# Kernel tuning notes

Hardware: AMD Instinct MI355X
Metric: run time of the kernel (lower is better)

## Reference

```python
import jax, jax.numpy as jnp
import numpy as np

B, N, D = 2, 4096, 1024
DS = 1024           # state_dim (defaults to embed_dim)
H = 4096            # mlp hidden = int(embed_dim * 4.0)
EPS = 1e-5


def _layernorm(x, w, b):
    mu = jnp.mean(x, axis=-1, keepdims=True)
    var = jnp.mean((x - mu) ** 2, axis=-1, keepdims=True)
    return (x - mu) * jax.lax.rsqrt(var + EPS) * w + b


def _selective_scan(deltaA, deltaB_u):
    # deltaA: (B, N, 1), deltaB_u: (B, N, DS). Recurrence h_i = dA_i * h + dBu_i.
    def step(h, inp):
        dA, dBu = inp           # (B,1), (B,DS)
        h = dA * h + dBu
        return h, h
    h0 = jnp.zeros((deltaB_u.shape[0], deltaB_u.shape[2]), deltaB_u.dtype)
    _, ys = jax.lax.scan(step, h0,
                         (jnp.swapaxes(deltaA, 0, 1), jnp.swapaxes(deltaB_u, 0, 1)))
    return jnp.swapaxes(ys, 0, 1)   # (B, N, DS)


def _forward(x, norm1_w, norm1_b, gate_w, gate_b, state_w, state_b,
             out_w, out_b, norm2_w, norm2_b, mlp_w1, mlp_b1, mlp_w2, mlp_b2):
    xn = _layernorm(x, norm1_w, norm1_b)
    g = xn @ gate_w + gate_b                       # (B,N,2D)
    gate, gate_gate = jnp.split(g, 2, axis=-1)
    gate = jax.nn.silu(gate)
    gate_gate = jax.nn.silu(gate_gate)
    u = (xn * gate) @ state_w + state_b            # (B,N,DS)
    Bm = gate_gate @ state_w + state_b             # (B,N,DS)
    # A = -ones(DS) -> delta*A = -delta broadcast over DS; keep (B,N,1)
    delta = jax.nn.softplus(jnp.mean(xn @ state_w + state_b, axis=-1, keepdims=True))
    deltaA = jnp.exp(-delta)                       # (B,N,1)
    deltaB_u = delta * Bm * u                      # (B,N,DS)
    # C = ones -> y_i = C_i * h_i = h_i
    y = _selective_scan(deltaA, deltaB_u)
    ssm_out = y @ out_w + out_b
    x = x + ssm_out
    x2 = _layernorm(x, norm2_w, norm2_b)
    mlp = jax.nn.gelu(x2 @ mlp_w1 + mlp_b1, approximate=False) @ mlp_w2 + mlp_b2
    return x + mlp


def setup_inputs() -> dict:
    key = jax.random.key(0)
    ks = jax.random.split(key, 12)
    s = 0.02
    p = lambda k, shape: jax.random.normal(k, shape, jnp.float32) * s
    return {
        "x": jax.random.normal(ks[0], (B, N, D), jnp.float32),
        "norm1_w": jnp.ones((D,), jnp.float32), "norm1_b": jnp.zeros((D,), jnp.float32),
        "gate_w": p(ks[1], (D, 2 * D)), "gate_b": p(ks[2], (2 * D,)),
        "state_w": p(ks[3], (D, DS)), "state_b": p(ks[4], (DS,)),
        "out_w": p(ks[5], (DS, D)), "out_b": p(ks[6], (D,)),
        "norm2_w": jnp.ones((D,), jnp.float32), "norm2_b": jnp.zeros((D,), jnp.float32),
        "mlp_w1": p(ks[7], (D, H)), "mlp_b1": p(ks[8], (H,)),
        "mlp_w2": p(ks[9], (H, D)), "mlp_b2": p(ks[10], (D,)),
    }


def reference(x, norm1_w, norm1_b, gate_w, gate_b, state_w, state_b,
              out_w, out_b, norm2_w, norm2_b, mlp_w1, mlp_b1, mlp_w2, mlp_b2):
    return _forward(x, norm1_w, norm1_b, gate_w, gate_b, state_w, state_b,
                    out_w, out_b, norm2_w, norm2_b, mlp_w1, mlp_b1, mlp_w2, mlp_b2)
```

## Files before the change

### kernel.cpp

```cpp
#include <hip/hip_runtime.h>
#include <hip/hip_bf16.h>
#include <math.h>

#define B_   2
#define N_   4096
#define D_   1024
#define DS_  1024
#define HID_ 4096
#define ROWS (B_ * N_)

#define CHK 128
#define TCH 32

typedef __attribute__((ext_vector_type(8))) short bf16x8;
typedef __attribute__((ext_vector_type(4))) float f32x4;

#define ASG __attribute__((address_space(1)))
#define AS3 __attribute__((address_space(3)))

__device__ __forceinline__ float bf2f(unsigned short u) {
  union { float f; unsigned int i; } v; v.i = ((unsigned int)u) << 16; return v.f;
}
__device__ __forceinline__ unsigned short f2bf(float f) {
  union { float f; unsigned int i; } v; v.f = f;
  unsigned int r = v.i + 0x7fffu + ((v.i >> 16) & 1u);
  return (unsigned short)(r >> 16);
}

__global__ void means_kernel(const float* __restrict__ W, const float* __restrict__ bvec,
                             float* __restrict__ swmean, float* __restrict__ sbmean) {
  __shared__ float sm[4];
  int bid = blockIdx.x, t = threadIdx.x;
  const float* src = (bid < D_) ? (W + (size_t)bid * DS_) : bvec;
  float s = 0.f;
  for (int j = t; j < DS_; j += 256) s += src[j];
  for (int o = 32; o; o >>= 1) s += __shfl_down(s, o);
  if ((t & 63) == 0) sm[t >> 6] = s;
  __syncthreads();
  if (t == 0) {
    float r = (sm[0] + sm[1] + sm[2] + sm[3]) * (1.f / DS_);
    if (bid < D_) swmean[bid] = r; else sbmean[0] = r;
  }
}

__global__ void transpose_bf16_kernel(const float* __restrict__ W, unsigned short* __restrict__ WT,
                                      int K, int N) {
  __shared__ float tile[32][33];
  int tx = threadIdx.x & 31, ty = threadIdx.x >> 5;
  int bn = blockIdx.x * 32, bk = blockIdx.y * 32;
  for (int i = ty; i < 32; i += 8)
    tile[i][tx] = W[(size_t)(bk + i) * N + bn + tx];
  __syncthreads();
  for (int i = ty; i < 32; i += 8)
    WT[(size_t)(bn + i) * K + bk + tx] = f2bf(tile[tx][i]);
}

template<bool WITH_DELTA>
__global__ void ln_kernel(const float* __restrict__ x, const float* __restrict__ w,
                          const float* __restrict__ bb, unsigned short* __restrict__ out_bf,
                          const float* __restrict__ swmean, const float* __restrict__ sbmean,
                          float* __restrict__ delta) {
  __shared__ float sm[8];
  __shared__ float bc[2];
  int row = blockIdx.x, t = threadIdx.x;
  const float* xr = x + (size_t)row * D_;
  float4 xv = ((const float4*)xr)[t];
  float s  = xv.x + xv.y + xv.z + xv.w;
  float sq = xv.x * xv.x + xv.y * xv.y + xv.z * xv.z + xv.w * xv.w;
  for (int o = 32; o; o >>= 1) { s += __shfl_down(s, o); sq += __shfl_down(sq, o); }
  if ((t & 63) == 0) { sm[t >> 6] = s; sm[4 + (t >> 6)] = sq; }
  __syncthreads();
  if (t == 0) {
    float ts = sm[0] + sm[1] + sm[2] + sm[3];
    float tq = sm[4] + sm[5] + sm[6] + sm[7];
    float mu = ts * (1.f / D_);
    float var = tq * (1.f / D_) - mu * mu;
    bc[0] = mu; bc[1] = rsqrtf(var + 1e-5f);
  }
  __syncthreads();
  float mu = bc[0], rs = bc[1];
  float4 wv = ((const float4*)w)[t];
  float4 bv = ((const float4*)bb)[t];
  float n0 = (xv.x - mu) * rs * wv.x + bv.x;
  float n1 = (xv.y - mu) * rs * wv.y + bv.y;
  float n2 = (xv.z - mu) * rs * wv.z + bv.z;
  float n3 = (xv.w - mu) * rs * wv.w + bv.w;
  ushort4 o4; o4.x = f2bf(n0); o4.y = f2bf(n1); o4.z = f2bf(n2); o4.w = f2bf(n3);
  ((ushort4*)(out_bf + (size_t)row * D_))[t] = o4;
  if (WITH_DELTA) {
    float4 sw = ((const float4*)swmean)[t];
    float d = n0 * sw.x + n1 * sw.y + n2 * sw.z + n3 * sw.w;
    for (int o = 32; o; o >>= 1) d += __shfl_down(d, o);
    if ((t & 63) == 0) sm[t >> 6] = d;
    __syncthreads();
    if (t == 0) {
      float z = sm[0] + sm[1] + sm[2] + sm[3] + sbmean[0];
      delta[row] = (z > 15.f) ? z : log1pf(__expf(z));
    }
  }
}


#define BARX { __builtin_amdgcn_s_barrier(); __builtin_amdgcn_sched_barrier(0); }

#define RD_A(TAU, H) { const char* ab_ = smem + ((((TAU)&1)*2+(H))<<14); \
  _Pragma("unroll") for (int mm_ = 0; mm_ < MB_H; ++mm_) \
  _Pragma("unroll") for (int ks_ = 0; ks_ < 2; ++ks_) { \
    int r_ = wr*(16*MB_H) + mm_*16 + l15; \
    int by_ = r_*128 + ks_*64 + kq16; by_ ^= ((by_>>7)&7)<<4; \
    af[mm_][ks_] = *(const bf16x8*)(ab_ + by_); } }

#define RD_B(TAU, H, DST) { const char* bb_ = smemB + ((((TAU)&1)*2+(H)))*SB; \
  _Pragma("unroll") for (int nn_ = 0; nn_ < NB_H; ++nn_) \
  _Pragma("unroll") for (int ks_ = 0; ks_ < 2; ++ks_) { \
    int r_ = wc*(16*NB_H) + nn_*16 + l15; \
    int by_ = r_*128 + ks_*64 + kq16; by_ ^= ((by_>>7)&7)<<4; \
    DST[nn_][ks_] = *(const bf16x8*)(bb_ + by_); } }

#define MFMAQ(QA, QB, BF) { __builtin_amdgcn_s_setprio(1); \
  _Pragma("unroll") for (int m_ = 0; m_ < MB_H; ++m_) \
  _Pragma("unroll") for (int n_ = 0; n_ < NB_H; ++n_) \
  _Pragma("unroll") for (int k_ = 0; k_ < 2; ++k_) \
    acc[(QA)*MB_H+m_][(QB)*NB_H+n_] = __builtin_amdgcn_mfma_f32_16x16x32_bf16( \
        af[m_][k_], BF[n_][k_], acc[(QA)*MB_H+m_][(QB)*NB_H+n_], 0, 0, 0); \
  __builtin_amdgcn_s_setprio(0); }

template<int BN, int EPI>
__global__ __launch_bounds__(512, 2) void gemm8p(
    const unsigned short* __restrict__ A1p, int lda1, int M1,
    const unsigned short* __restrict__ A2p, int lda2,
    const unsigned short* __restrict__ BT, const float* __restrict__ bias,
    void* __restrict__ Cout, const float* __restrict__ res,
    int N, int K, int nbx) {
  constexpr int WN   = (BN == 256) ? 4 : 2;
  constexpr int MB_H = (BN == 256) ? 4 : 2;
  constexpr int NB_H = 2;
  constexpr int MF   = 2 * MB_H;
  constexpr int LB   = BN / 128;
  constexpr int SB   = (BN / 2) * 64 * 2;
  __shared__ char smem[65536 + 4 * SB];
  char* smemB = smem + 65536;

  const int nwg = gridDim.x;
  int bid = blockIdx.x;
  int wg = (bid & 7) * (nwg >> 3) + (bid >> 3);
  const int bx = wg % nbx, by = wg / nbx;
  const int mbase = by * 256, nbase = bx * BN;

  const int tid = threadIdx.x;
  const int lane = tid & 63, wid = tid >> 6;
  const int wr = wid / WN, wc = wid % WN;
  const int l15 = lane & 15, kq16 = (lane >> 4) * 16;
  const int wvoff16 = wid << 10;

  const unsigned short* Ause; int ldaU;
  if (mbase < M1) { Ause = A1p + (size_t)mbase * lda1; ldaU = lda1; }
  else            { Ause = A2p + (size_t)(mbase - M1) * lda2; ldaU = lda2; }

  int L0 = tid * 16;        int b0 = L0 ^ (((L0 >> 7) & 7) << 4);
  int L1 = 8192 + tid * 16; int b1 = L1 ^ (((L1 >> 7) & 7) << 4);
  const unsigned short* pA0 = Ause + (size_t)(b0 >> 7) * ldaU + ((b0 & 127) >> 1);
  const unsigned short* pA1 = Ause + (size_t)(b1 >> 7) * ldaU + ((b1 & 127) >> 1);
  const unsigned short* pB0 = BT + (size_t)(nbase + (b0 >> 7)) * K + ((b0 & 127) >> 1);
  const unsigned short* pB1 = BT + (size_t)(nbase + (b1 >> 7)) * K + ((b1 & 127) >> 1);

  auto stageA = [&](int tau, int h, bool en) {
    if (!en) return;
    char* l0 = smem + (((tau & 1) * 2 + h) << 14) + wvoff16;
    const unsigned short* g0 = pA0 + (size_t)h * 128 * ldaU + tau * 64;
    const unsigned short* g1 = pA1 + (size_t)h * 128 * ldaU + tau * 64;
    __builtin_amdgcn_global_load_lds((const ASG void*)g0, (AS3 void*)l0, 16, 0, 0);
    __builtin_amdgcn_global_load_lds((const ASG void*)g1, (AS3 void*)(l0 + 8192), 16, 0, 0);
  };
  auto stageB = [&](int tau, int h, bool en) {
    if (!en) return;
    char* l0 = smemB + ((tau & 1) * 2 + h) * SB + wvoff16;
    const unsigned short* g0 = pB0 + (size_t)h * (BN / 2) * K + tau * 64;
    __builtin_amdgcn_global_load_lds((const ASG void*)g0, (AS3 void*)l0, 16, 0, 0);
    if constexpr (LB == 2) {
      const unsigned short* g1 = pB1 + (size_t)h * (BN / 2) * K + tau * 64;
      __builtin_amdgcn_global_load_lds((const ASG void*)g1, (AS3 void*)(l0 + 8192), 16, 0, 0);
    }
  };
  auto vm_steady = [&]() {
    if constexpr (BN == 256) { asm volatile("s_waitcnt vmcnt(6)" ::: "memory"); }
    else                     { asm volatile("s_waitcnt vmcnt(5)" ::: "memory"); }
  };

  f32x4 acc[MF][4];
#pragma unroll
  for (int m = 0; m < MF; ++m)
#pragma unroll
    for (int n = 0; n < 4; ++n) acc[m][n] = (f32x4){0.f, 0.f, 0.f, 0.f};
  bf16x8 af[MB_H][2], bq0[NB_H][2], bq1[NB_H][2];

  const int NT = K >> 6, NI = NT >> 1;

  stageA(0, 0, true); stageB(0, 0, true); stageA(0, 1, true); stageB(0, 1, true);
  stageA(1, 0, true); stageB(1, 0, true); stageA(1, 1, true);
  vm_steady();
  BARX;

#pragma unroll 1
  for (int i = 0; i < NI; ++i) {
    const int t0 = 2 * i;
    const bool st = (i < NI - 1);
    RD_A(t0, 0); RD_B(t0, 0, bq0); stageB(t0 + 1, 1, true);
    BARX; MFMAQ(0, 0, bq0); BARX;
    RD_B(t0, 1, bq1); stageA(t0 + 2, 0, st);
    BARX; MFMAQ(0, 1, bq1); BARX;
    RD_A(t0, 1); stageB(t0 + 2, 0, st);
    BARX; MFMAQ(1, 1, bq1); BARX;
    stageA(t0 + 2, 1, st);
    if (st) { vm_steady(); } else { asm volatile("s_waitcnt vmcnt(0)" ::: "memory"); }
    BARX; MFMAQ(1, 0, bq0); BARX;
    RD_A(t0 + 1, 0); RD_B(t0 + 1, 0, bq0); stageB(t0 + 2, 1, st);
    BARX; MFMAQ(0, 0, bq0); BARX;
    RD_B(t0 + 1, 1, bq1); stageA(t0 + 3, 0, st);
    BARX; MFMAQ(0, 1, bq1); BARX;
    RD_A(t0 + 1, 1); stageB(t0 + 3, 0, st);
    BARX; MFMAQ(1, 1, bq1); BARX;
    stageA(t0 + 3, 1, st);
    if (st) vm_steady();
    BARX; MFMAQ(1, 0, bq0); BARX;
  }

#pragma unroll
  for (int mb = 0; mb < MF; ++mb) {
    int row = mbase + wr * (16 * MB_H) + (mb % MB_H) * 16 + (mb / MB_H) * 128 + (lane >> 4) * 4;
#pragma unroll
    for (int nb = 0; nb < 4; ++nb) {
      int col = nbase + wc * (16 * NB_H) + (nb % NB_H) * 16 + (nb / NB_H) * (BN / 2) + l15;
      float bc = bias[col];
#pragma unroll
      for (int r = 0; r < 4; ++r) {
        float v = acc[mb][nb][r] + bc;
        size_t off = (size_t)(row + r) * N + col;
        if (EPI == 1) {
          v = v / (1.f + __expf(-v));
          ((unsigned short*)Cout)[off] = f2bf(v);
        } else if (EPI == 2) {
          ((unsigned short*)Cout)[off] = f2bf(v);
        } else if (EPI == 3) {
          ((float*)Cout)[off] = v + res[off];
        } else if (EPI == 4) {
          float tt = v * (0.7978845608f + 0.0356774081f * v * v);
          v = v / (1.f + __expf(-2.f * tt));
          ((unsigned short*)Cout)[off] = f2bf(v);
        }
      }
    }
  }
}

__global__ void ew_xg_kernel(const unsigned short* __restrict__ xn,
                             const unsigned short* __restrict__ gs,
                             unsigned short* __restrict__ xg) {
  size_t i8 = ((size_t)blockIdx.x * 256 + threadIdx.x) * 8;
  size_t row = i8 >> 10, col = i8 & 1023;
  uint4 xv = *(const uint4*)(xn + i8);
  uint4 gv = *(const uint4*)(gs + row * 2048 + col);
  const unsigned short* xs = (const unsigned short*)&xv;
  const unsigned short* gg = (const unsigned short*)&gv;
  uint4 ov; unsigned short* o = (unsigned short*)&ov;
#pragma unroll
  for (int j = 0; j < 8; ++j) o[j] = f2bf(bf2f(xs[j]) * bf2f(gg[j]));
  *(uint4*)(xg + i8) = ov;
}

__global__ void ew_dbu_kernel(const unsigned short* __restrict__ u,
                              const unsigned short* __restrict__ bm,
                              const float* __restrict__ delta,
                              unsigned short* __restrict__ dbu) {
  size_t i8 = ((size_t)blockIdx.x * 256 + threadIdx.x) * 8;
  size_t row = i8 >> 10;
  float dl = delta[row];
  uint4 uv = *(const uint4*)(u + i8);
  uint4 bv = *(const uint4*)(bm + i8);
  const unsigned short* us = (const unsigned short*)&uv;
  const unsigned short* bs = (const unsigned short*)&bv;
  uint4 ov; unsigned short* o = (unsigned short*)&ov;
#pragma unroll
  for (int j = 0; j < 8; ++j) o[j] = f2bf(dl * bf2f(us[j]) * bf2f(bs[j]));
  *(uint4*)(dbu + i8) = ov;
}

__global__ void scan_a_kernel(const unsigned short* __restrict__ dbu,
                              const float* __restrict__ delta,
                              float* __restrict__ hend, float* __restrict__ S) {
  int blk = blockIdx.x;
  int b = blk / CHK, c = blk % CHK;
  int ch = threadIdx.x;
  const unsigned short* p = dbu + ((size_t)(b * N_ + c * TCH)) * DS_ + ch;
  const float* dp = delta + b * N_ + c * TCH;
  float h = 0.f, dsum = 0.f;
#pragma unroll 4
  for (int t = 0; t < TCH; ++t) {
    float dl = dp[t];
    h = __expf(-dl) * h + bf2f(p[(size_t)t * DS_]);
    dsum += dl;
  }
  hend[(size_t)blk * DS_ + ch] = h;
  if (ch == 0) S[blk] = dsum;
}

__global__ void scan_combine_kernel(const float* __restrict__ hend, const float* __restrict__ S,
                                    float* __restrict__ carryin) {
  int b = blockIdx.x, ch = threadIdx.x;
  float carry = 0.f;
  for (int c = 0; c < CHK; ++c) {
    size_t o = (size_t)(b * CHK + c) * DS_ + ch;
    carryin[o] = carry;
    carry = __expf(-S[b * CHK + c]) * carry + hend[o];
  }
}

__global__ void scan_b_kernel(const unsigned short* __restrict__ dbu,
                              const float* __restrict__ delta,
                              const float* __restrict__ carryin,
                              unsigned short* __restrict__ y) {
  int blk = blockIdx.x;
  int b = blk / CHK, c = blk % CHK;
  int ch = threadIdx.x;
  size_t base = ((size_t)(b * N_ + c * TCH)) * DS_ + ch;
  const float* dp = delta + b * N_ + c * TCH;
  float h = carryin[(size_t)blk * DS_ + ch];
#pragma unroll 4
  for (int t = 0; t < TCH; ++t) {
    h = __expf(-dp[t]) * h + bf2f(dbu[base + (size_t)t * DS_]);
    y[base + (size_t)t * DS_] = f2bf(h);
  }
}

extern "C" void kernel_launch(void* const* d_in, const int* in_sizes, int n_in,
                              void* d_out, int out_size, void* d_ws, size_t ws_size,
                              hipStream_t stream) {
  const float* x       = (const float*)d_in[0];
  const float* n1w     = (const float*)d_in[1];
  const float* n1b     = (const float*)d_in[2];
  const float* gate_w  = (const float*)d_in[3];
  const float* gate_b  = (const float*)d_in[4];
  const float* state_w = (const float*)d_in[5];
  const float* state_b = (const float*)d_in[6];
  const float* out_w   = (const float*)d_in[7];
  const float* out_b   = (const float*)d_in[8];
  const float* n2w     = (const float*)d_in[9];
  const float* n2b     = (const float*)d_in[10];
  const float* mlp_w1  = (const float*)d_in[11];
  const float* mlp_b1  = (const float*)d_in[12];
  const float* mlp_w2  = (const float*)d_in[13];
  const float* mlp_b2  = (const float*)d_in[14];
  float* outp = (float*)d_out;

  char* w = (char*)d_ws;
  size_t off = 0;
  auto alloc = [&](size_t bytes) { char* p = w + off; off += (bytes + 255) & ~(size_t)255; return p; };

  unsigned short* gate_wT  = (unsigned short*)alloc((size_t)2048 * 1024 * 2);
  unsigned short* state_wT = (unsigned short*)alloc((size_t)1024 * 1024 * 2);
  unsigned short* out_wT   = (unsigned short*)alloc((size_t)1024 * 1024 * 2);
  unsigned short* w1T      = (unsigned short*)alloc((size_t)4096 * 1024 * 2);
  unsigned short* w2T      = (unsigned short*)alloc((size_t)1024 * 4096 * 2);
  float* swmean  = (float*)alloc(D_ * 4);
  float* sbmean  = (float*)alloc(256);
  float* delta   = (float*)alloc((size_t)ROWS * 4);
  float* hend    = (float*)alloc((size_t)B_ * CHK * DS_ * 4);
  float* carryin = (float*)alloc((size_t)B_ * CHK * DS_ * 4);
  float* S       = (float*)alloc((size_t)B_ * CHK * 4);
  unsigned short* xn = (unsigned short*)alloc((size_t)ROWS * D_ * 2);
  unsigned short* gs = (unsigned short*)alloc((size_t)ROWS * HID_ * 2);
  unsigned short* xg = (unsigned short*)alloc((size_t)ROWS * D_ * 2);
  float* x1          = (float*)alloc((size_t)ROWS * D_ * 4);

  unsigned short* dbu = xn;
  unsigned short* h1  = gs;
  unsigned short* y   = xg;
  unsigned short* x2  = xg;
  unsigned short* u   = (unsigned short*)x1;
  unsigned short* bm  = u + (size_t)ROWS * D_;

  means_kernel<<<D_ + 1, 256, 0, stream>>>(state_w, state_b, swmean, sbmean);
  transpose_bf16_kernel<<<dim3(2048 / 32, 1024 / 32), 256, 0, stream>>>(gate_w, gate_wT, 1024, 2048);
  transpose_bf16_kernel<<<dim3(1024 / 32, 1024 / 32), 256, 0, stream>>>(state_w, state_wT, 1024, 1024);
  transpose_bf16_kernel<<<dim3(1024 / 32, 1024 / 32), 256, 0, stream>>>(out_w, out_wT, 1024, 1024);
  transpose_bf16_kernel<<<dim3(4096 / 32, 1024 / 32), 256, 0, stream>>>(mlp_w1, w1T, 1024, 4096);
  transpose_bf16_kernel<<<dim3(1024 / 32, 4096 / 32), 256, 0, stream>>>(mlp_w2, w2T, 4096, 1024);

  ln_kernel<true><<<ROWS, 256, 0, stream>>>(x, n1w, n1b, xn, swmean, sbmean, delta);

  const int BIG = 1 << 30;
  gemm8p<256, 1><<<256, 512, 0, stream>>>(xn, 1024, BIG, xn, 1024,
                                          gate_wT, gate_b, gs, nullptr, 2048, 1024, 8);
  ew_xg_kernel<<<(ROWS * D_) / 8 / 256, 256, 0, stream>>>(xn, gs, xg);
  gemm8p<256, 2><<<256, 512, 0, stream>>>(xg, 1024, 8192, gs + 1024, 2048,
                                          state_wT, state_b, u, nullptr, 1024, 1024, 4);
  ew_dbu_kernel<<<(ROWS * D_) / 8 / 256, 256, 0, stream>>>(u, bm, delta, dbu);

  scan_a_kernel<<<B_ * CHK, 1024, 0, stream>>>(dbu, delta, hend, S);
  scan_combine_kernel<<<B_, 1024, 0, stream>>>(hend, S, carryin);
  scan_b_kernel<<<B_ * CHK, 1024, 0, stream>>>(dbu, delta, carryin, y);

  gemm8p<128, 3><<<256, 512, 0, stream>>>(y, 1024, BIG, y, 1024,
                                          out_wT, out_b, x1, x, 1024, 1024, 8);
  ln_kernel<false><<<ROWS, 256, 0, stream>>>(x1, n2w, n2b, x2, nullptr, nullptr, nullptr);
  gemm8p<256, 4><<<512, 512, 0, stream>>>(x2, 1024, BIG, x2, 1024,
                                          w1T, mlp_b1, h1, nullptr, 4096, 1024, 16);
  gemm8p<128, 3><<<256, 512, 0, stream>>>(h1, 4096, BIG, h1, 4096,
                                          w2T, mlp_b2, outp, x1, 1024, 4096, 8);
}
```

Measured before the change: 367.4 us.

## Fuse xn*gate product into gate GEMM epilogue and relax barrier scheduling

Adds an EPI==5 epilogue to the gate GEMM that applies SiLU and writes the first half multiplied by xn directly into xg, and the second half as a compact 1024-wide gate_gate buffer. This removes the separate ew_xg kernel and the 2048-wide gs round trip, and the state GEMM now reads a contiguous gate_gate array. It also drops sched_barrier from the barrier macro and issues global stage loads before the LDS reads in each phase, letting the compiler interleave instructions more freely. The risk is that the compiler reorders LDS reads or MFMAs across the barriers in ways that hurt the hand-tuned pipeline.

Result: slower. 392.9 us (+6.9%).

```diff
diff --git a/kernel.cpp b/kernel.cpp
--- a/kernel.cpp
+++ b/kernel.cpp
@@ -101,7 +101,7 @@
 }
 
 
-#define BARX { __builtin_amdgcn_s_barrier(); __builtin_amdgcn_sched_barrier(0); }
+#define BAR __builtin_amdgcn_s_barrier()
 
 #define RD_A(TAU, H) { const char* ab_ = smem + ((((TAU)&1)*2+(H))<<14); \
   _Pragma("unroll") for (int mm_ = 0; mm_ < MB_H; ++mm_) \
@@ -131,7 +131,7 @@
     const unsigned short* __restrict__ A2p, int lda2,
     const unsigned short* __restrict__ BT, const float* __restrict__ bias,
     void* __restrict__ Cout, const float* __restrict__ res,
-    int N, int K, int nbx) {
+    int N, int K, int nbx, void* __restrict__ Cout2) {
   constexpr int WN   = (BN == 256) ? 4 : 2;
   constexpr int MB_H = (BN == 256) ? 4 : 2;
   constexpr int NB_H = 2;
@@ -199,30 +199,30 @@
   stageA(0, 0, true); stageB(0, 0, true); stageA(0, 1, true); stageB(0, 1, true);
   stageA(1, 0, true); stageB(1, 0, true); stageA(1, 1, true);
   vm_steady();
-  BARX;
+  BAR;
 
 #pragma unroll 1
   for (int i = 0; i < NI; ++i) {
     const int t0 = 2 * i;
     const bool st = (i < NI - 1);
-    RD_A(t0, 0); RD_B(t0, 0, bq0); stageB(t0 + 1, 1, true);
-    BARX; MFMAQ(0, 0, bq0); BARX;
-    RD_B(t0, 1, bq1); stageA(t0 + 2, 0, st);
-    BARX; MFMAQ(0, 1, bq1); BARX;
-    RD_A(t0, 1); stageB(t0 + 2, 0, st);
-    BARX; MFMAQ(1, 1, bq1); BARX;
+    stageB(t0 + 1, 1, true); RD_A(t0, 0); RD_B(t0, 0, bq0);
+    BAR; MFMAQ(0, 0, bq0); BAR;
+    stageA(t0 + 2, 0, st); RD_B(t0, 1, bq1);
+    BAR; MFMAQ(0, 1, bq1); BAR;
+    stageB(t0 + 2, 0, st); RD_A(t0, 1);
+    BAR; MFMAQ(1, 1, bq1); BAR;
     stageA(t0 + 2, 1, st);
     if (st) { vm_steady(); } else { asm volatile("s_waitcnt vmcnt(0)" ::: "memory"); }
-    BARX; MFMAQ(1, 0, bq0); BARX;
-    RD_A(t0 + 1, 0); RD_B(t0 + 1, 0, bq0); stageB(t0 + 2, 1, st);
-    BARX; MFMAQ(0, 0, bq0); BARX;
-    RD_B(t0 + 1, 1, bq1); stageA(t0 + 3, 0, st);
-    BARX; MFMAQ(0, 1, bq1); BARX;
-    RD_A(t0 + 1, 1); stageB(t0 + 3, 0, st);
-    BARX; MFMAQ(1, 1, bq1); BARX;
+    BAR; MFMAQ(1, 0, bq0); BAR;
+    stageB(t0 + 2, 1, st); RD_A(t0 + 1, 0); RD_B(t0 + 1, 0, bq0);
+    BAR; MFMAQ(0, 0, bq0); BAR;
+    stageA(t0 + 3, 0, st); RD_B(t0 + 1, 1, bq1);
+    BAR; MFMAQ(0, 1, bq1); BAR;
+    stageB(t0 + 3, 0, st); RD_A(t0 + 1, 1);
+    BAR; MFMAQ(1, 1, bq1); BAR;
     stageA(t0 + 3, 1, st);
     if (st) vm_steady();
-    BARX; MFMAQ(1, 0, bq0); BARX;
+    BAR; MFMAQ(1, 0, bq0); BAR;
   }
 
 #pragma unroll
@@ -247,25 +247,20 @@
           float tt = v * (0.7978845608f + 0.0356774081f * v * v);
           v = v / (1.f + __expf(-2.f * tt));
           ((unsigned short*)Cout)[off] = f2bf(v);
+        } else if (EPI == 5) {
+          float s = v / (1.f + __expf(-v));
+          if (col < 1024) {
+            size_t o1 = (size_t)(row + r) * 1024 + col;
+            float xv = bf2f(((const unsigned short*)res)[o1]);
+            ((unsigned short*)Cout)[o1] = f2bf(s * xv);
+          } else {
+            size_t o2 = (size_t)(row + r) * 1024 + (col - 1024);
+            ((unsigned short*)Cout2)[o2] = f2bf(s);
+          }
         }
       }
     }
   }
-}
-
-__global__ void ew_xg_kernel(const unsigned short* __restrict__ xn,
-                             const unsigned short* __restrict__ gs,
-                             unsigned short* __restrict__ xg) {
-  size_t i8 = ((size_t)blockIdx.x * 256 + threadIdx.x) * 8;
-  size_t row = i8 >> 10, col = i8 & 1023;
-  uint4 xv = *(const uint4*)(xn + i8);
-  uint4 gv = *(const uint4*)(gs + row * 2048 + col);
-  const unsigned short* xs = (const unsigned short*)&xv;
-  const unsigned short* gg = (const unsigned short*)&gv;
-  uint4 ov; unsigned short* o = (unsigned short*)&ov;
-#pragma unroll
-  for (int j = 0; j < 8; ++j) o[j] = f2bf(bf2f(xs[j]) * bf2f(gg[j]));
-  *(uint4*)(xg + i8) = ov;
 }
 
 __global__ void ew_dbu_kernel(const unsigned short* __restrict__ u,
@@ -372,12 +367,13 @@
   unsigned short* xg = (unsigned short*)alloc((size_t)ROWS * D_ * 2);
   float* x1          = (float*)alloc((size_t)ROWS * D_ * 4);
 
-  unsigned short* dbu = xn;
-  unsigned short* h1  = gs;
-  unsigned short* y   = xg;
-  unsigned short* x2  = xg;
-  unsigned short* u   = (unsigned short*)x1;
-  unsigned short* bm  = u + (size_t)ROWS * D_;
+  unsigned short* dbu   = xn;
+  unsigned short* gsil2 = gs;
+  unsigned short* h1    = gs;
+  unsigned short* y     = xg;
+  unsigned short* x2    = xg;
+  unsigned short* u     = (unsigned short*)x1;
+  unsigned short* bm    = u + (size_t)ROWS * D_;
 
   means_kernel<<<D_ + 1, 256, 0, stream>>>(state_w, state_b, swmean, sbmean);
   transpose_bf16_kernel<<<dim3(2048 / 32, 1024 / 32), 256, 0, stream>>>(gate_w, gate_wT, 1024, 2048);
@@ -389,11 +385,10 @@
   ln_kernel<true><<<ROWS, 256, 0, stream>>>(x, n1w, n1b, xn, swmean, sbmean, delta);
 
   const int BIG = 1 << 30;
-  gemm8p<256, 1><<<256, 512, 0, stream>>>(xn, 1024, BIG, xn, 1024,
-                                          gate_wT, gate_b, gs, nullptr, 2048, 1024, 8);
-  ew_xg_kernel<<<(ROWS * D_) / 8 / 256, 256, 0, stream>>>(xn, gs, xg);
-  gemm8p<256, 2><<<256, 512, 0, stream>>>(xg, 1024, 8192, gs + 1024, 2048,
-                                          state_wT, state_b, u, nullptr, 1024, 1024, 4);
+  gemm8p<256, 5><<<256, 512, 0, stream>>>(xn, 1024, BIG, xn, 1024,
+                                          gate_wT, gate_b, xg, (const float*)xn, 2048, 1024, 8, gsil2);
+  gemm8p<256, 2><<<256, 512, 0, stream>>>(xg, 1024, 8192, gsil2, 1024,
+                                          state_wT, state_b, u, nullptr, 1024, 1024, 4, nullptr);
   ew_dbu_kernel<<<(ROWS * D_) / 8 / 256, 256, 0, stream>>>(u, bm, delta, dbu);
 
   scan_a_kernel<<<B_ * CHK, 1024, 0, stream>>>(dbu, delta, hend, S);
@@ -401,10 +396,10 @@
   scan_b_kernel<<<B_ * CHK, 1024, 0, stream>>>(dbu, delta, carryin, y);
 
   gemm8p<128, 3><<<256, 512, 0, stream>>>(y, 1024, BIG, y, 1024,
-                                          out_wT, out_b, x1, x, 1024, 1024, 8);
+                                          out_wT, out_b, x1, x, 1024, 1024, 8, nullptr);
   ln_kernel<false><<<ROWS, 256, 0, stream>>>(x1, n2w, n2b, x2, nullptr, nullptr, nullptr);
   gemm8p<256, 4><<<512, 512, 0, stream>>>(x2, 1024, BIG, x2, 1024,
-                                          w1T, mlp_b1, h1, nullptr, 4096, 1024, 16);
+                                          w1T, mlp_b1, h1, nullptr, 4096, 1024, 16, nullptr);
   gemm8p<128, 3><<<256, 512, 0, stream>>>(h1, 4096, BIG, h1, 4096,
-                                          w2T, mlp_b2, outp, x1, 1024, 4096, 8);
-}
+                                          w2T, mlp_b2, outp, x1, 1024, 4096, 8, nullptr);
+}
```

## Fuse delta*B*u into scan kernels and make MLP1 GEMM persistent over two tiles

Applied to the files above, without the earlier changes.

The elementwise dbu kernel is removed. Both scan passes now read u and Bm directly and compute delta*Bm*u inline, which saves one full write and read of an intermediate. The MLP up-projection GEMM gets a P2 mode in which each of 256 workgroups computes two M tiles back to back, continuing the load pipeline across the tile boundary and running the epilogue in between. The sched_barrier after each s_barrier is also dropped, giving the compiler more scheduling freedom but possibly disturbing the hand-tuned interleave; the scans now read two bf16 streams instead of one.

Measured after the change: 406.5 us. 10.6% more time.

```diff
diff --git a/kernel.cpp b/kernel.cpp
--- a/kernel.cpp
+++ b/kernel.cpp
@@ -101,7 +101,7 @@
 }
 
 
-#define BARX { __builtin_amdgcn_s_barrier(); __builtin_amdgcn_sched_barrier(0); }
+#define BAR __builtin_amdgcn_s_barrier()
 
 #define RD_A(TAU, H) { const char* ab_ = smem + ((((TAU)&1)*2+(H))<<14); \
   _Pragma("unroll") for (int mm_ = 0; mm_ < MB_H; ++mm_) \
@@ -125,7 +125,7 @@
         af[m_][k_], BF[n_][k_], acc[(QA)*MB_H+m_][(QB)*NB_H+n_], 0, 0, 0); \
   __builtin_amdgcn_s_setprio(0); }
 
-template<int BN, int EPI>
+template<int BN, int EPI, bool P2>
 __global__ __launch_bounds__(512, 2) void gemm8p(
     const unsigned short* __restrict__ A1p, int lda1, int M1,
     const unsigned short* __restrict__ A2p, int lda2,
@@ -146,6 +146,7 @@
   int wg = (bid & 7) * (nwg >> 3) + (bid >> 3);
   const int bx = wg % nbx, by = wg / nbx;
   const int mbase = by * 256, nbase = bx * BN;
+  const int mstep = (nwg / nbx) * 256;
 
   const int tid = threadIdx.x;
   const int lane = tid & 63, wid = tid >> 6;
@@ -156,6 +157,7 @@
   const unsigned short* Ause; int ldaU;
   if (mbase < M1) { Ause = A1p + (size_t)mbase * lda1; ldaU = lda1; }
   else            { Ause = A2p + (size_t)(mbase - M1) * lda2; ldaU = lda2; }
+  const size_t A2off = (size_t)mstep * ldaU;
 
   int L0 = tid * 16;        int b0 = L0 ^ (((L0 >> 7) & 7) << 4);
   int L1 = 8192 + tid * 16; int b1 = L1 ^ (((L1 >> 7) & 7) << 4);
@@ -164,17 +166,27 @@
   const unsigned short* pB0 = BT + (size_t)(nbase + (b0 >> 7)) * K + ((b0 & 127) >> 1);
   const unsigned short* pB1 = BT + (size_t)(nbase + (b1 >> 7)) * K + ((b1 & 127) >> 1);
 
-  auto stageA = [&](int tau, int h, bool en) {
-    if (!en) return;
-    char* l0 = smem + (((tau & 1) * 2 + h) << 14) + wvoff16;
-    const unsigned short* g0 = pA0 + (size_t)h * 128 * ldaU + tau * 64;
-    const unsigned short* g1 = pA1 + (size_t)h * 128 * ldaU + tau * 64;
+  const int KT  = K >> 6;
+  const int NI1 = KT >> 1;
+  const int NTV = P2 ? 2 * KT : KT;
+  const int NIV = P2 ? 2 * NI1 : NI1;
+
+  auto stageA = [&](int tau, int h) {
+    if (tau >= NTV) return;
+    int slot = tau & 1;
+    const unsigned short *a0 = pA0, *a1 = pA1;
+    if (P2 && tau >= KT) { tau -= KT; a0 += A2off; a1 += A2off; }
+    char* l0 = smem + ((slot * 2 + h) << 14) + wvoff16;
+    const unsigned short* g0 = a0 + (size_t)h * 128 * ldaU + tau * 64;
+    const unsigned short* g1 = a1 + (size_t)h * 128 * ldaU + tau * 64;
     __builtin_amdgcn_global_load_lds((const ASG void*)g0, (AS3 void*)l0, 16, 0, 0);
     __builtin_amdgcn_global_load_lds((const ASG void*)g1, (AS3 void*)(l0 + 8192), 16, 0, 0);
   };
-  auto stageB = [&](int tau, int h, bool en) {
-    if (!en) return;
-    char* l0 = smemB + ((tau & 1) * 2 + h) * SB + wvoff16;
+  auto stageB = [&](int tau, int h) {
+    if (tau >= NTV) return;
+    int slot = tau & 1;
+    if (P2 && tau >= KT) tau -= KT;
+    char* l0 = smemB + (slot * 2 + h) * SB + wvoff16;
     const unsigned short* g0 = pB0 + (size_t)h * (BN / 2) * K + tau * 64;
     __builtin_amdgcn_global_load_lds((const ASG void*)g0, (AS3 void*)l0, 16, 0, 0);
     if constexpr (LB == 2) {
@@ -194,63 +206,72 @@
     for (int n = 0; n < 4; ++n) acc[m][n] = (f32x4){0.f, 0.f, 0.f, 0.f};
   bf16x8 af[MB_H][2], bq0[NB_H][2], bq1[NB_H][2];
 
-  const int NT = K >> 6, NI = NT >> 1;
-
-  stageA(0, 0, true); stageB(0, 0, true); stageA(0, 1, true); stageB(0, 1, true);
-  stageA(1, 0, true); stageB(1, 0, true); stageA(1, 1, true);
-  vm_steady();
-  BARX;
-
-#pragma unroll 1
-  for (int i = 0; i < NI; ++i) {
-    const int t0 = 2 * i;
-    const bool st = (i < NI - 1);
-    RD_A(t0, 0); RD_B(t0, 0, bq0); stageB(t0 + 1, 1, true);
-    BARX; MFMAQ(0, 0, bq0); BARX;
-    RD_B(t0, 1, bq1); stageA(t0 + 2, 0, st);
-    BARX; MFMAQ(0, 1, bq1); BARX;
-    RD_A(t0, 1); stageB(t0 + 2, 0, st);
-    BARX; MFMAQ(1, 1, bq1); BARX;
-    stageA(t0 + 2, 1, st);
-    if (st) { vm_steady(); } else { asm volatile("s_waitcnt vmcnt(0)" ::: "memory"); }
-    BARX; MFMAQ(1, 0, bq0); BARX;
-    RD_A(t0 + 1, 0); RD_B(t0 + 1, 0, bq0); stageB(t0 + 2, 1, st);
-    BARX; MFMAQ(0, 0, bq0); BARX;
-    RD_B(t0 + 1, 1, bq1); stageA(t0 + 3, 0, st);
-    BARX; MFMAQ(0, 1, bq1); BARX;
-    RD_A(t0 + 1, 1); stageB(t0 + 3, 0, st);
-    BARX; MFMAQ(1, 1, bq1); BARX;
-    stageA(t0 + 3, 1, st);
-    if (st) vm_steady();
-    BARX; MFMAQ(1, 0, bq0); BARX;
-  }
-
-#pragma unroll
-  for (int mb = 0; mb < MF; ++mb) {
-    int row = mbase + wr * (16 * MB_H) + (mb % MB_H) * 16 + (mb / MB_H) * 128 + (lane >> 4) * 4;
-#pragma unroll
-    for (int nb = 0; nb < 4; ++nb) {
-      int col = nbase + wc * (16 * NB_H) + (nb % NB_H) * 16 + (nb / NB_H) * (BN / 2) + l15;
-      float bc = bias[col];
-#pragma unroll
-      for (int r = 0; r < 4; ++r) {
-        float v = acc[mb][nb][r] + bc;
-        size_t off = (size_t)(row + r) * N + col;
-        if (EPI == 1) {
-          v = v / (1.f + __expf(-v));
-          ((unsigned short*)Cout)[off] = f2bf(v);
-        } else if (EPI == 2) {
-          ((unsigned short*)Cout)[off] = f2bf(v);
-        } else if (EPI == 3) {
-          ((float*)Cout)[off] = v + res[off];
-        } else if (EPI == 4) {
-          float tt = v * (0.7978845608f + 0.0356774081f * v * v);
-          v = v / (1.f + __expf(-2.f * tt));
-          ((unsigned short*)Cout)[off] = f2bf(v);
+  auto epi = [&](int tile) {
+    const int moff = P2 ? tile * mstep : 0;
+#pragma unroll
+    for (int mb = 0; mb < MF; ++mb) {
+      int row = mbase + moff + wr * (16 * MB_H) + (mb % MB_H) * 16 + (mb / MB_H) * 128 + (lane >> 4) * 4;
+#pragma unroll
+      for (int nb = 0; nb < 4; ++nb) {
+        int col = nbase + wc * (16 * NB_H) + (nb % NB_H) * 16 + (nb / NB_H) * (BN / 2) + l15;
+        float bc = bias[col];
+#pragma unroll
+        for (int r = 0; r < 4; ++r) {
+          float v = acc[mb][nb][r] + bc;
+          size_t off = (size_t)(row + r) * N + col;
+          if (EPI == 1) {
+            v = v / (1.f + __expf(-v));
+            ((unsigned short*)Cout)[off] = f2bf(v);
+          } else if (EPI == 2) {
+            ((unsigned short*)Cout)[off] = f2bf(v);
+          } else if (EPI == 3) {
+            ((float*)Cout)[off] = v + res[off];
+          } else if (EPI == 4) {
+            float tt = v * (0.7978845608f + 0.0356774081f * v * v);
+            v = v / (1.f + __expf(-2.f * tt));
+            ((unsigned short*)Cout)[off] = f2bf(v);
+          }
         }
       }
     }
-  }
+  };
+
+  stageA(0, 0); stageB(0, 0); stageA(0, 1); stageB(0, 1);
+  stageA(1, 0); stageB(1, 0); stageA(1, 1);
+  vm_steady();
+  BAR;
+
+#pragma unroll 1
+  for (int vi = 0; vi < NIV; ++vi) {
+    const int t0 = 2 * vi;
+    stageB(t0 + 1, 1); RD_A(t0, 0); RD_B(t0, 0, bq0);
+    BAR; MFMAQ(0, 0, bq0); BAR;
+    stageA(t0 + 2, 0); RD_B(t0, 1, bq1);
+    BAR; MFMAQ(0, 1, bq1); BAR;
+    stageB(t0 + 2, 0); RD_A(t0, 1);
+    BAR; MFMAQ(1, 1, bq1); BAR;
+    stageA(t0 + 2, 1);
+    if (t0 + 2 < NTV) { vm_steady(); } else { asm volatile("s_waitcnt vmcnt(0)" ::: "memory"); }
+    BAR; MFMAQ(1, 0, bq0); BAR;
+    stageB(t0 + 2, 1); RD_A(t0 + 1, 0); RD_B(t0 + 1, 0, bq0);
+    BAR; MFMAQ(0, 0, bq0); BAR;
+    stageA(t0 + 3, 0); RD_B(t0 + 1, 1, bq1);
+    BAR; MFMAQ(0, 1, bq1); BAR;
+    stageB(t0 + 3, 0); RD_A(t0 + 1, 1);
+    BAR; MFMAQ(1, 1, bq1); BAR;
+    stageA(t0 + 3, 1);
+    if (t0 + 2 < NTV) vm_steady();
+    BAR; MFMAQ(1, 0, bq0); BAR;
+    if (P2 && vi == NI1 - 1) {
+      epi(0);
+#pragma unroll
+      for (int m = 0; m < MF; ++m)
+#pragma unroll
+        for (int n = 0; n < 4; ++n) acc[m][n] = (f32x4){0.f, 0.f, 0.f, 0.f};
+    }
+  }
+
+  epi(P2 ? 1 : 0);
 }
 
 __global__ void ew_xg_kernel(const unsigned short* __restrict__ xn,
@@ -268,36 +289,21 @@
   *(uint4*)(xg + i8) = ov;
 }
 
-__global__ void ew_dbu_kernel(const unsigned short* __restrict__ u,
+__global__ void scan_a_kernel(const unsigned short* __restrict__ u,
                               const unsigned short* __restrict__ bm,
-                              const float* __restrict__ delta,
-                              unsigned short* __restrict__ dbu) {
-  size_t i8 = ((size_t)blockIdx.x * 256 + threadIdx.x) * 8;
-  size_t row = i8 >> 10;
-  float dl = delta[row];
-  uint4 uv = *(const uint4*)(u + i8);
-  uint4 bv = *(const uint4*)(bm + i8);
-  const unsigned short* us = (const unsigned short*)&uv;
-  const unsigned short* bs = (const unsigned short*)&bv;
-  uint4 ov; unsigned short* o = (unsigned short*)&ov;
-#pragma unroll
-  for (int j = 0; j < 8; ++j) o[j] = f2bf(dl * bf2f(us[j]) * bf2f(bs[j]));
-  *(uint4*)(dbu + i8) = ov;
-}
-
-__global__ void scan_a_kernel(const unsigned short* __restrict__ dbu,
                               const float* __restrict__ delta,
                               float* __restrict__ hend, float* __restrict__ S) {
   int blk = blockIdx.x;
   int b = blk / CHK, c = blk % CHK;
   int ch = threadIdx.x;
-  const unsigned short* p = dbu + ((size_t)(b * N_ + c * TCH)) * DS_ + ch;
+  size_t base = ((size_t)(b * N_ + c * TCH)) * DS_ + ch;
   const float* dp = delta + b * N_ + c * TCH;
   float h = 0.f, dsum = 0.f;
 #pragma unroll 4
   for (int t = 0; t < TCH; ++t) {
     float dl = dp[t];
-    h = __expf(-dl) * h + bf2f(p[(size_t)t * DS_]);
+    float du = dl * bf2f(u[base + (size_t)t * DS_]) * bf2f(bm[base + (size_t)t * DS_]);
+    h = __expf(-dl) * h + du;
     dsum += dl;
   }
   hend[(size_t)blk * DS_ + ch] = h;
@@ -315,7 +321,8 @@
   }
 }
 
-__global__ void scan_b_kernel(const unsigned short* __restrict__ dbu,
+__global__ void scan_b_kernel(const unsigned short* __restrict__ u,
+                              const unsigned short* __restrict__ bm,
                               const float* __restrict__ delta,
                               const float* __restrict__ carryin,
                               unsigned short* __restrict__ y) {
@@ -327,7 +334,9 @@
   float h = carryin[(size_t)blk * DS_ + ch];
 #pragma unroll 4
   for (int t = 0; t < TCH; ++t) {
-    h = __expf(-dp[t]) * h + bf2f(dbu[base + (size_t)t * DS_]);
+    float dl = dp[t];
+    float du = dl * bf2f(u[base + (size_t)t * DS_]) * bf2f(bm[base + (size_t)t * DS_]);
+    h = __expf(-dl) * h + du;
     y[base + (size_t)t * DS_] = f2bf(h);
   }
 }
@@ -372,12 +381,11 @@
   unsigned short* xg = (unsigned short*)alloc((size_t)ROWS * D_ * 2);
   float* x1          = (float*)alloc((size_t)ROWS * D_ * 4);
 
-  unsigned short* dbu = xn;
-  unsigned short* h1  = gs;
-  unsigned short* y   = xg;
-  unsigned short* x2  = xg;
-  unsigned short* u   = (unsigned short*)x1;
-  unsigned short* bm  = u + (size_t)ROWS * D_;
+  unsigned short* h1 = gs;
+  unsigned short* y  = xg;
+  unsigned short* x2 = xg;
+  unsigned short* u  = (unsigned short*)x1;
+  unsigned short* bm = u + (size_t)ROWS * D_;
 
   means_kernel<<<D_ + 1, 256, 0, stream>>>(state_w, state_b, swmean, sbmean);
   transpose_bf16_kernel<<<dim3(2048 / 32, 1024 / 32), 256, 0, stream>>>(gate_w, gate_wT, 1024, 2048);
@@ -389,22 +397,21 @@
   ln_kernel<true><<<ROWS, 256, 0, stream>>>(x, n1w, n1b, xn, swmean, sbmean, delta);
 
   const int BIG = 1 << 30;
-  gemm8p<256, 1><<<256, 512, 0, stream>>>(xn, 1024, BIG, xn, 1024,
-                                          gate_wT, gate_b, gs, nullptr, 2048, 1024, 8);
+  gemm8p<256, 1, false><<<256, 512, 0, stream>>>(xn, 1024, BIG, xn, 1024,
+                                                 gate_wT, gate_b, gs, nullptr, 2048, 1024, 8);
   ew_xg_kernel<<<(ROWS * D_) / 8 / 256, 256, 0, stream>>>(xn, gs, xg);
-  gemm8p<256, 2><<<256, 512, 0, stream>>>(xg, 1024, 8192, gs + 1024, 2048,
-                                          state_wT, state_b, u, nullptr, 1024, 1024, 4);
-  ew_dbu_kernel<<<(ROWS * D_) / 8 / 256, 256, 0, stream>>>(u, bm, delta, dbu);
-
-  scan_a_kernel<<<B_ * CHK, 1024, 0, stream>>>(dbu, delta, hend, S);
+  gemm8p<256, 2, false><<<256, 512, 0, stream>>>(xg, 1024, 8192, gs + 1024, 2048,
+                                                 state_wT, state_b, u, nullptr, 1024, 1024, 4);
+
+  scan_a_kernel<<<B_ * CHK, 1024, 0, stream>>>(u, bm, delta, hend, S);
   scan_combine_kernel<<<B_, 1024, 0, stream>>>(hend, S, carryin);
-  scan_b_kernel<<<B_ * CHK, 1024, 0, stream>>>(dbu, delta, carryin, y);
-
-  gemm8p<128, 3><<<256, 512, 0, stream>>>(y, 1024, BIG, y, 1024,
-                                          out_wT, out_b, x1, x, 1024, 1024, 8);
+  scan_b_kernel<<<B_ * CHK, 1024, 0, stream>>>(u, bm, delta, carryin, y);
+
+  gemm8p<128, 3, false><<<256, 512, 0, stream>>>(y, 1024, BIG, y, 1024,
+                                                 out_wT, out_b, x1, x, 1024, 1024, 8);
   ln_kernel<false><<<ROWS, 256, 0, stream>>>(x1, n2w, n2b, x2, nullptr, nullptr, nullptr);
-  gemm8p<256, 4><<<512, 512, 0, stream>>>(x2, 1024, BIG, x2, 1024,
-                                          w1T, mlp_b1, h1, nullptr, 4096, 1024, 16);
-  gemm8p<128, 3><<<256, 512, 0, stream>>>(h1, 4096, BIG, h1, 4096,
-                                          w2T, mlp_b2, outp, x1, 1024, 4096, 8);
-}
+  gemm8p<256, 4, true><<<256, 512, 0, stream>>>(x2, 1024, BIG, x2, 1024,
+                                                w1T, mlp_b1, h1, nullptr, 4096, 1024, 16);
+  gemm8p<128, 3, false><<<256, 512, 0, stream>>>(h1, 4096, BIG, h1, 4096,
+                                                 w2T, mlp_b2, outp, x1, 1024, 4096, 8);
+}
```
